# Optimization experiments

Measured on AMD Instinct MI355X. Metric: run time of the kernel, lower is better.

## Reference

```python
import jax, jax.numpy as jnp
import numpy as np

B, N1, N2, C2, K = 8, 2048, 128, 256, 3
D_POS, H0, H1 = 32, 512, 1024


def setup_inputs() -> dict:
    key = jax.random.key(0)
    ks = jax.random.split(key, 14)
    return {
        "xyz1": jax.random.normal(ks[0], (B, N1, 3), jnp.float32),
        "xyz2": jax.random.normal(ks[1], (B, N2, 3), jnp.float32),
        "feat2": jax.random.normal(ks[2], (B, N2, C2), jnp.float32),
        "lrf2": jax.random.normal(ks[3], (B, N2, 3, 3), jnp.float32),
        "w_pos": jax.random.normal(ks[4], (D_POS, 4), jnp.float32) * 0.1,
        "pos_scale": jax.random.uniform(ks[5], (D_POS,), jnp.float32, 0.5, 1.5),
        "pos_bias": jax.random.normal(ks[6], (D_POS,), jnp.float32) * 0.1,
        "w0": jax.random.normal(ks[7], (H0, C2 + D_POS), jnp.float32) * 0.05,
        "s0": jax.random.uniform(ks[8], (H0,), jnp.float32, 0.5, 1.5),
        "b0": jax.random.normal(ks[9], (H0,), jnp.float32) * 0.1,
        "w1": jax.random.normal(ks[10], (H1, H0), jnp.float32) * 0.04,
        "s1": jax.random.uniform(ks[11], (H1,), jnp.float32, 0.5, 1.5),
        "b1": jax.random.normal(ks[12], (H1,), jnp.float32) * 0.1,
        "k": K,
    }


def reference(xyz1, xyz2, feat2, lrf2, w_pos, pos_scale, pos_bias,
              w0, s0, b0, w1, s1, b1, k):
    Bb = xyz1.shape[0]
    # --- get_dists: full pairwise sqrt-distance matrix (B, N1, N2) ---
    d2 = (jnp.sum(xyz1 * xyz1, -1)[:, :, None]
          + jnp.sum(xyz2 * xyz2, -1)[:, None, :]
          - 2.0 * jnp.einsum('bmc,bnc->bmn', xyz1, xyz2))
    dists = jnp.sqrt(jnp.where(d2 < 0, 1e-7, d2))
    # --- k-NN: smallest k in ascending order (== torch.sort then slice) ---
    _, inds = jax.lax.top_k(-dists, k)                    # (B, N1, k)
    bidx = jnp.arange(Bb)[:, None, None]
    feat_nb = feat2[bidx, inds]                           # (B, N1, k, C2)
    close = xyz2[bidx, inds]                              # (B, N1, k, 3)
    lrf_nb = lrf2[bidx, inds]                             # (B, N1, k, 3, 3)
    # --- geometric angle embedding ---
    rel = xyz1[:, :, None, :] - close                     # (B, N1, k, 3)
    rel_norm = jnp.linalg.norm(rel, axis=-1)              # (B, N1, k)
    unit = rel / jnp.maximum(rel_norm, 1e-12)[..., None]  # F.normalize eps
    angle = jnp.einsum('bnkij,bnkj->bnki', lrf_nb, unit)  # (B, N1, k, 3)
    rp = jnp.concatenate([rel_norm[..., None], angle], -1)  # (B, N1, k, 4)
    # --- posembed: 1x1 Conv2d (no bias) + folded BN + LeakyReLU(0.2) ---
    pos = jax.nn.leaky_relu(
        jnp.einsum('bnkc,oc->bnko', rp, w_pos) * pos_scale + pos_bias, 0.2)
    # --- backbone: two 1x1 convs with folded BN + ReLU ---
    x = jnp.concatenate([feat_nb, pos], -1)               # (B, N1, k, C2+32)
    h0 = jax.nn.relu(jnp.einsum('bnkc,oc->bnko', x, w0) * s0 + b0)
    h1 = jax.nn.relu(jnp.einsum('bnkc,oc->bnko', h0, w1) * s1 + b1)
    # --- sum over neighbors, return (B, C_out, N1) like torch ---
    return jnp.transpose(jnp.sum(h1, axis=2), (0, 2, 1))
```

## Files before the change

kernel.cpp:

```cpp
#include <hip/hip_runtime.h>


typedef unsigned short u16;
typedef __bf16 bf16x8 __attribute__((ext_vector_type(8)));
typedef float f32x4 __attribute__((ext_vector_type(4)));
typedef u16 u16x4 __attribute__((ext_vector_type(4)));

#define BQ 8
#define N1Q 2048
#define N2Q 128
#define C2Q 256
#define DPOS 32
#define H0Q 512
#define H1Q 1024
#define NQ (BQ * N1Q)

#define WS_W0F 0u
#define WS_W0P 262144u
#define WS_W1 294912u
#define WS_F2B 1343488u
#define WS_F 1867776u
#define WS_H0 3964928u

__device__ __forceinline__ u16 f2bf(float f) {
  unsigned int u = __builtin_bit_cast(unsigned int, f);
  return (u16)((u + 0x7FFFu + ((u >> 16) & 1u)) >> 16);
}

__device__ __forceinline__ void load16_lds(const void* g, void* l) {
  __builtin_amdgcn_global_load_lds(
      (const __attribute__((address_space(1))) unsigned int*)g,
      (__attribute__((address_space(3))) unsigned int*)l, 16, 0, 0);
}

__global__ void convert_inputs(const float* __restrict__ w0,
                               const float* __restrict__ w1,
                               const float* __restrict__ feat2,
                               u16* __restrict__ w0f, u16* __restrict__ w0p,
                               u16* __restrict__ w1b, u16* __restrict__ f2b) {
  int i = blockIdx.x * 256 + threadIdx.x;
  if (i < 131072) {
    int h = i >> 8, c = i & 255;
    w0f[i] = f2bf(w0[h * 288 + c]);
  } else if (i < 147456) {
    int j = i - 131072;
    int h = j >> 5, c = j & 31;
    w0p[j] = f2bf(w0[h * 288 + 256 + c]);
  } else if (i < 671744) {
    int j = i - 147456;
    w1b[j] = f2bf(w1[j]);
  } else {
    int j = i - 671744;
    f2b[j] = f2bf(feat2[j]);
  }
}

__global__ __launch_bounds__(256, 2) void fgemm(const u16* __restrict__ A,
                                                const u16* __restrict__ W,
                                                float* __restrict__ F) {
  __shared__ alignas(16) u16 As[128 * 32];
  __shared__ alignas(16) u16 Bs[128 * 32];
  const int m0 = (blockIdx.x >> 2) * 128, n0 = (blockIdx.x & 3) * 128;
  const int t = threadIdx.x;
  const int wv = t >> 6, lane = t & 63;
  const int wm = wv >> 1, wn = wv & 1;
  const int quad = lane >> 4, cc = lane & 15;
  const int srow = lane & 15, skc = quad * 8;
  f32x4 acc[4][4] = {};

  for (int k0 = 0; k0 < 256; k0 += 32) {
#pragma unroll
    for (int i = 0; i < 2; i++) {
      int g = i * 4 + wv;
      load16_lds(A + (size_t)(m0 + g * 16 + srow) * 256 + k0 + skc,
                 (char*)As + g * 1024 + (lane << 4));
      load16_lds(W + (size_t)(n0 + g * 16 + srow) * 256 + k0 + skc,
                 (char*)Bs + g * 1024 + (lane << 4));
    }
    __syncthreads();
    bf16x8 af[4], bf[4];
#pragma unroll
    for (int mt = 0; mt < 4; mt++)
      af[mt] = *(const bf16x8*)((const char*)As + (wm * 4 + mt) * 1024 + (lane << 4));
#pragma unroll
    for (int nt = 0; nt < 4; nt++)
      bf[nt] = *(const bf16x8*)((const char*)Bs + (wn * 4 + nt) * 1024 + (lane << 4));
#pragma unroll
    for (int mt = 0; mt < 4; mt++)
#pragma unroll
      for (int nt = 0; nt < 4; nt++)
        acc[mt][nt] = __builtin_amdgcn_mfma_f32_16x16x32_bf16(
            af[mt], bf[nt], acc[mt][nt], 0, 0, 0);
    __syncthreads();
  }

#pragma unroll
  for (int nt = 0; nt < 4; nt++) {
    int gn = n0 + wn * 64 + nt * 16 + cc;
#pragma unroll
    for (int mt = 0; mt < 4; mt++) {
      int gm = m0 + wm * 64 + mt * 16 + quad * 4;
#pragma unroll
      for (int r = 0; r < 4; r++)
        F[(size_t)(gm + r) * H0Q + gn] = acc[mt][nt][r];
    }
  }
}

__global__ __launch_bounds__(256, 2) void build_h0(
    const float* __restrict__ xyz1, const float* __restrict__ xyz2,
    const float* __restrict__ lrf2, const float* __restrict__ w_pos,
    const float* __restrict__ pscale, const float* __restrict__ pbias,
    const u16* __restrict__ w0p, const float* __restrict__ F,
    const float* __restrict__ s0, const float* __restrict__ b0,
    u16* __restrict__ H0) {
  __shared__ float xyz2s[N2Q * 3];
  __shared__ float n2s[N2Q];
  __shared__ float lrfs[N2Q * 9];
  __shared__ float wps[DPOS * 4];
  __shared__ float pss[DPOS];
  __shared__ float pbs[DPOS];
  __shared__ int idxb[192];
  __shared__ float candd[64 * 13];
  __shared__ int candi[64 * 13];
  __shared__ alignas(16) u16 posb[12 * 512];

  const int t = threadIdx.x;
  const int qb = blockIdx.x * 64;
  const int b = qb >> 11;

  for (int i = t; i < N2Q * 3; i += 256) xyz2s[i] = xyz2[b * N2Q * 3 + i];
  for (int i = t; i < N2Q * 9; i += 256) lrfs[i] = lrf2[b * N2Q * 9 + i];
  if (t < DPOS * 4) wps[t] = w_pos[t];
  if (t < DPOS) { pss[t] = pscale[t]; pbs[t] = pbias[t]; }
  __syncthreads();
  if (t < N2Q) {
    float x = xyz2s[t * 3], y = xyz2s[t * 3 + 1], z = xyz2s[t * 3 + 2];
    n2s[t] = x * x + y * y + z * z;
  }
  __syncthreads();

  {
    const int ql = t >> 2, qt = t & 3;
    const int q = qb + ql;
    const float px = xyz1[q * 3], py = xyz1[q * 3 + 1], pz = xyz1[q * 3 + 2];
    const float pn = px * px + py * py + pz * pz;
    float d0 = 1e30f, d1 = 1e30f, d2v = 1e30f;
    int i0 = 0, i1 = 0, i2 = 0;
    const int ibeg = qt * 32;
    for (int i = ibeg; i < ibeg + 32; i++) {
      float dt = px * xyz2s[i * 3] + py * xyz2s[i * 3 + 1] + pz * xyz2s[i * 3 + 2];
      float d = pn + n2s[i] - 2.f * dt;
      if (d < d0) {
        d2v = d1; i2 = i1; d1 = d0; i1 = i0; d0 = d; i0 = i;
      } else if (d < d1) {
        d2v = d1; i2 = i1; d1 = d; i1 = i;
      } else if (d < d2v) {
        d2v = d; i2 = i;
      }
    }
    int base = ql * 13 + qt * 3;
    candd[base] = d0;      candi[base] = i0;
    candd[base + 1] = d1;  candi[base + 1] = i1;
    candd[base + 2] = d2v; candi[base + 2] = i2;
  }
  __syncthreads();

  if (t < 64) {
    float d0 = 1e30f, d1 = 1e30f, d2v = 1e30f;
    int i0 = 0, i1 = 0, i2 = 0;
    int base = t * 13;
#pragma unroll
    for (int c = 0; c < 12; c++) {
      float d = candd[base + c];
      int id = candi[base + c];
      if (d < d0) {
        d2v = d1; i2 = i1; d1 = d0; i1 = i0; d0 = d; i0 = id;
      } else if (d < d1) {
        d2v = d1; i2 = i1; d1 = d; i1 = id;
      } else if (d < d2v) {
        d2v = d; i2 = id;
      }
    }
    idxb[t] = i0;
    idxb[64 + t] = i1;
    idxb[128 + t] = i2;
  }
  __syncthreads();

  if (t < 192) {
    const int ql = t & 63;
    const int q = qb + ql;
    const float px = xyz1[q * 3], py = xyz1[q * 3 + 1], pz = xyz1[q * 3 + 2];
    const int id = idxb[t];
    float rx = px - xyz2s[id * 3];
    float ry = py - xyz2s[id * 3 + 1];
    float rz = pz - xyz2s[id * 3 + 2];
    float rn = sqrtf(rx * rx + ry * ry + rz * rz);
    float inv = 1.f / fmaxf(rn, 1e-12f);
    float ux = rx * inv, uy = ry * inv, uz = rz * inv;
    const float* L = lrfs + id * 9;
    float a0 = L[0] * ux + L[1] * uy + L[2] * uz;
    float a1 = L[3] * ux + L[4] * uy + L[5] * uz;
    float a2 = L[6] * ux + L[7] * uy + L[8] * uz;
    u16* pd = posb + (t >> 4) * 512 + (t & 15) * 8;
#pragma unroll
    for (int o = 0; o < DPOS; o++) {
      float v = wps[o * 4] * rn + wps[o * 4 + 1] * a0 + wps[o * 4 + 2] * a1 +
                wps[o * 4 + 3] * a2;
      v = v * pss[o] + pbs[o];
      v = (v >= 0.f) ? v : 0.2f * v;
      pd[(o >> 3) * 128 + (o & 7)] = f2bf(v);
    }
  }
  __syncthreads();

  const int wv = t >> 6, lane = t & 63;
  const int quad = lane >> 4, cc = lane & 15;
  const float* Fr[3];
  u16* Hr[3];
#pragma unroll
  for (int mt = 0; mt < 3; mt++) {
    int rl = wv * 48 + mt * 16 + cc;
    Fr[mt] = F + ((size_t)(b * N2Q + idxb[rl])) * H0Q;
    int jj = rl >> 6, ql = rl & 63;
    Hr[mt] = H0 + ((size_t)(jj * NQ) + qb + ql) * H0Q;
  }
  bf16x8 afr[3];
#pragma unroll
  for (int mt = 0; mt < 3; mt++)
    afr[mt] = *(const bf16x8*)((const char*)posb + (wv * 3 + mt) * 1024 + (lane << 4));
  const f32x4 zf = {};
  for (int n0 = 0; n0 < H0Q; n0 += 128) {
    bf16x8 bfr[8];
#pragma unroll
    for (int nt = 0; nt < 8; nt++)
      bfr[nt] = *(const bf16x8*)(w0p + (n0 + nt * 16 + cc) * 32 + quad * 8);
    f32x4 acc[3][8];
#pragma unroll
    for (int mt = 0; mt < 3; mt++)
#pragma unroll
      for (int nt = 0; nt < 8; nt++)
        acc[mt][nt] = __builtin_amdgcn_mfma_f32_16x16x32_bf16(bfr[nt], afr[mt],
                                                              zf, 0, 0, 0);
#pragma unroll
    for (int nt = 0; nt < 8; nt++) {
      int hb = n0 + nt * 16 + quad * 4;
      f32x4 sv = *(const f32x4*)(s0 + hb);
      f32x4 bvv = *(const f32x4*)(b0 + hb);
#pragma unroll
      for (int mt = 0; mt < 3; mt++) {
        f32x4 fv = *(const f32x4*)(Fr[mt] + hb);
        u16x4 o4;
#pragma unroll
        for (int r = 0; r < 4; r++) {
          float h = (fv[r] + acc[mt][nt][r]) * sv[r] + bvv[r];
          h = h > 0.f ? h : 0.f;
          o4[r] = f2bf(h);
        }
        *(u16x4*)(Hr[mt] + hb) = o4;
      }
    }
  }
}

__global__ __launch_bounds__(512, 2) void gemm2(const u16* __restrict__ A,
                                                const u16* __restrict__ W,
                                                const float* __restrict__ s,
                                                const float* __restrict__ bz,
                                                float* __restrict__ out) {
  __shared__ alignas(16) u16 As[3][128 * 64];
  __shared__ alignas(16) u16 Bs[3][256 * 64];
  const int id = blockIdx.x;
  const int xcd = id & 7, g = id >> 3;
  const int m0 = (xcd * 16 + (g >> 2)) * 128;
  const int n0 = (g & 3) * 256;
  const int t = threadIdx.x;
  const int wv = t >> 6, lane = t & 63;
  const int wm = wv >> 2, wn = wv & 3;
  const int quad = lane >> 4, cc = lane & 15;
  const int lr = lane & 15, lk = (lane >> 4) * 8;

  const size_t aOff = (size_t)(m0 + wv * 16 + lr) * 512 + lk;
  const size_t bOff = (size_t)(n0 + wv * 32 + lr) * 512 + lk;

  float sv[4], bv[4];
#pragma unroll
  for (int nt = 0; nt < 4; nt++) {
    int gn = n0 + wn * 64 + nt * 16 + cc;
    sv[nt] = s[gn];
    bv[nt] = bz[gn];
  }

  auto stage = [&](int kt, int bi) {
    const u16* Ap = A + (size_t)(kt >> 3) * ((size_t)NQ * H0Q) + ((kt & 7) << 6);
    const u16* Wp = W + ((kt & 7) << 6);
    char* ab = (char*)As[bi] + (lane << 4);
    char* bb = (char*)Bs[bi] + (lane << 4);
    load16_lds(Ap + aOff, ab + wv * 1024);
    load16_lds(Ap + aOff + 32, ab + (8 + wv) * 1024);
    load16_lds(Wp + bOff, bb + (wv * 2) * 1024);
    load16_lds(Wp + bOff + (size_t)16 * 512, bb + (wv * 2 + 1) * 1024);
    load16_lds(Wp + bOff + 32, bb + (16 + wv * 2) * 1024);
    load16_lds(Wp + bOff + (size_t)16 * 512 + 32, bb + (16 + wv * 2 + 1) * 1024);
  };

  f32x4 sum[4][4] = {};
  f32x4 acc[4][4] = {};

  auto tile = [&](int bi, int ktStage) {
    bf16x8 af[2][4], bf[2][4];
    const char* ab = (const char*)As[bi] + (lane << 4);
    const char* bb = (const char*)Bs[bi] + (lane << 4);
#pragma unroll
    for (int kk = 0; kk < 2; kk++)
#pragma unroll
      for (int mt = 0; mt < 4; mt++)
        af[kk][mt] = *(const bf16x8*)(ab + (kk * 8 + wm * 4 + mt) * 1024);
#pragma unroll
    for (int kk = 0; kk < 2; kk++)
#pragma unroll
      for (int nt = 0; nt < 4; nt++)
        bf[kk][nt] = *(const bf16x8*)(bb + (kk * 16 + wn * 4 + nt) * 1024);
    asm volatile("s_waitcnt lgkmcnt(0)" ::: "memory");
    __builtin_amdgcn_s_barrier();
    if (ktStage >= 0) stage(ktStage, bi);
    __builtin_amdgcn_s_setprio(1);
#pragma unroll
    for (int kk = 0; kk < 2; kk++)
#pragma unroll
      for (int mt = 0; mt < 4; mt++)
#pragma unroll
        for (int nt = 0; nt < 4; nt++)
          acc[mt][nt] = __builtin_amdgcn_mfma_f32_16x16x32_bf16(
              af[kk][mt], bf[kk][nt], acc[mt][nt], 0, 0, 0);
    __builtin_amdgcn_s_setprio(0);
  };

  auto fold = [&]() {
#pragma unroll
    for (int mt = 0; mt < 4; mt++)
#pragma unroll
      for (int nt = 0; nt < 4; nt++) {
#pragma unroll
        for (int r = 0; r < 4; r++) {
          float h = acc[mt][nt][r] * sv[nt] + bv[nt];
          sum[mt][nt][r] += (h > 0.f ? h : 0.f);
        }
        acc[mt][nt] = f32x4{};
      }
  };

  stage(0, 0);
  stage(1, 1);
  stage(2, 2);

#pragma unroll 3
  for (int kt = 0; kt < 21; kt++) {
    asm volatile("s_waitcnt vmcnt(12)" ::: "memory");
    __builtin_amdgcn_s_barrier();
    tile(kt % 3, kt + 3);
    if ((kt & 7) == 7) fold();
  }
  asm volatile("s_waitcnt vmcnt(12)" ::: "memory");
  __builtin_amdgcn_s_barrier();
  tile(0, -1);
  asm volatile("s_waitcnt vmcnt(6)" ::: "memory");
  __builtin_amdgcn_s_barrier();
  tile(1, -1);
  asm volatile("s_waitcnt vmcnt(0)" ::: "memory");
  __builtin_amdgcn_s_barrier();
  tile(2, -1);
  fold();

#pragma unroll
  for (int nt = 0; nt < 4; nt++) {
    int gn = n0 + wn * 64 + nt * 16 + cc;
#pragma unroll
    for (int mt = 0; mt < 4; mt++) {
      int gm = m0 + wm * 64 + mt * 16 + quad * 4;
#pragma unroll
      for (int r = 0; r < 4; r++) {
        int q = gm + r;
        out[((size_t)(q >> 11) * H1Q + gn) * N1Q + (q & 2047)] = sum[mt][nt][r];
      }
    }
  }
}

extern "C" void kernel_launch(void* const* d_in, const int* in_sizes, int n_in,
                              void* d_out, int out_size, void* d_ws,
                              size_t ws_size, hipStream_t stream) {
  const float* xyz1 = (const float*)d_in[0];
  const float* xyz2 = (const float*)d_in[1];
  const float* feat2 = (const float*)d_in[2];
  const float* lrf2 = (const float*)d_in[3];
  const float* w_pos = (const float*)d_in[4];
  const float* pscale = (const float*)d_in[5];
  const float* pbias = (const float*)d_in[6];
  const float* w0 = (const float*)d_in[7];
  const float* s0 = (const float*)d_in[8];
  const float* b0 = (const float*)d_in[9];
  const float* w1 = (const float*)d_in[10];
  const float* s1 = (const float*)d_in[11];
  const float* b1 = (const float*)d_in[12];
  float* out = (float*)d_out;

  char* ws = (char*)d_ws;
  u16* w0f = (u16*)(ws + WS_W0F);
  u16* w0p = (u16*)(ws + WS_W0P);
  u16* w1b = (u16*)(ws + WS_W1);
  u16* f2b = (u16*)(ws + WS_F2B);
  float* F = (float*)(ws + WS_F);
  u16* H0 = (u16*)(ws + WS_H0);

  convert_inputs<<<933888 / 256, 256, 0, stream>>>(w0, w1, feat2, w0f, w0p,
                                                   w1b, f2b);
  fgemm<<<32, 256, 0, stream>>>(f2b, w0f, F);
  build_h0<<<NQ / 64, 256, 0, stream>>>(xyz1, xyz2, lrf2, w_pos, pscale,
                                        pbias, w0p, F, s0, b0, H0);
  gemm2<<<512, 512, 0, stream>>>(H0, w1b, s1, b1, out);
}
```

Measured before the change: 231.1 us.

## Split build_h0 across output column blocks and deepen gemm2 pipeline to six stages

```diff
diff --git a/kernel.cpp b/kernel.cpp
--- a/kernel.cpp
+++ b/kernel.cpp
@@ -128,6 +128,7 @@
   const int t = threadIdx.x;
   const int qb = blockIdx.x * 64;
   const int b = qb >> 11;
+  const int n0 = blockIdx.y << 7;
 
   for (int i = t; i < N2Q * 3; i += 256) xyz2s[i] = xyz2[b * N2Q * 3 + i];
   for (int i = t; i < N2Q * 9; i += 256) lrfs[i] = lrf2[b * N2Q * 9 + i];
@@ -231,35 +232,33 @@
   for (int mt = 0; mt < 3; mt++)
     afr[mt] = *(const bf16x8*)((const char*)posb + (wv * 3 + mt) * 1024 + (lane << 4));
   const f32x4 zf = {};
-  for (int n0 = 0; n0 < H0Q; n0 += 128) {
-    bf16x8 bfr[8];
+  bf16x8 bfr[8];
+#pragma unroll
+  for (int nt = 0; nt < 8; nt++)
+    bfr[nt] = *(const bf16x8*)(w0p + (n0 + nt * 16 + cc) * 32 + quad * 8);
+  f32x4 acc[3][8];
+#pragma unroll
+  for (int mt = 0; mt < 3; mt++)
 #pragma unroll
     for (int nt = 0; nt < 8; nt++)
-      bfr[nt] = *(const bf16x8*)(w0p + (n0 + nt * 16 + cc) * 32 + quad * 8);
-    f32x4 acc[3][8];
-#pragma unroll
-    for (int mt = 0; mt < 3; mt++)
-#pragma unroll
-      for (int nt = 0; nt < 8; nt++)
-        acc[mt][nt] = __builtin_amdgcn_mfma_f32_16x16x32_bf16(bfr[nt], afr[mt],
-                                                              zf, 0, 0, 0);
-#pragma unroll
-    for (int nt = 0; nt < 8; nt++) {
-      int hb = n0 + nt * 16 + quad * 4;
-      f32x4 sv = *(const f32x4*)(s0 + hb);
-      f32x4 bvv = *(const f32x4*)(b0 + hb);
-#pragma unroll
-      for (int mt = 0; mt < 3; mt++) {
-        f32x4 fv = *(const f32x4*)(Fr[mt] + hb);
-        u16x4 o4;
-#pragma unroll
-        for (int r = 0; r < 4; r++) {
-          float h = (fv[r] + acc[mt][nt][r]) * sv[r] + bvv[r];
-          h = h > 0.f ? h : 0.f;
-          o4[r] = f2bf(h);
-        }
-        *(u16x4*)(Hr[mt] + hb) = o4;
+      acc[mt][nt] = __builtin_amdgcn_mfma_f32_16x16x32_bf16(bfr[nt], afr[mt],
+                                                            zf, 0, 0, 0);
+#pragma unroll
+  for (int nt = 0; nt < 8; nt++) {
+    int hb = n0 + nt * 16 + quad * 4;
+    f32x4 sv = *(const f32x4*)(s0 + hb);
+    f32x4 bvv = *(const f32x4*)(b0 + hb);
+#pragma unroll
+    for (int mt = 0; mt < 3; mt++) {
+      f32x4 fv = *(const f32x4*)(Fr[mt] + hb);
+      u16x4 o4;
+#pragma unroll
+      for (int r = 0; r < 4; r++) {
+        float h = (fv[r] + acc[mt][nt][r]) * sv[r] + bvv[r];
+        h = h > 0.f ? h : 0.f;
+        o4[r] = f2bf(h);
       }
+      *(u16x4*)(Hr[mt] + hb) = o4;
     }
   }
 }
@@ -269,8 +268,8 @@
                                                 const float* __restrict__ s,
                                                 const float* __restrict__ bz,
                                                 float* __restrict__ out) {
-  __shared__ alignas(16) u16 As[3][128 * 64];
-  __shared__ alignas(16) u16 Bs[3][256 * 64];
+  __shared__ alignas(16) u16 As[6][128 * 32];
+  __shared__ alignas(16) u16 Bs[6][256 * 32];
   const int id = blockIdx.x;
   const int xcd = id & 7, g = id >> 3;
   const int m0 = (xcd * 16 + (g >> 2)) * 128;
@@ -281,59 +280,57 @@
   const int quad = lane >> 4, cc = lane & 15;
   const int lr = lane & 15, lk = (lane >> 4) * 8;
 
-  const size_t aOff = (size_t)(m0 + wv * 16 + lr) * 512 + lk;
-  const size_t bOff = (size_t)(n0 + wv * 32 + lr) * 512 + lk;
-
-  float sv[4], bv[4];
+  const size_t aBase = (size_t)(m0 + wv * 16 + lr) * 512 + lk;
+  const size_t bBase0 = (size_t)(n0 + wv * 32 + lr) * 512 + lk;
+  const size_t bBase1 = bBase0 + (size_t)16 * 512;
+  const int adst = wv * 1024 + (lane << 4);
+  const int bdst0 = (wv * 2) * 1024 + (lane << 4);
+  const int bdst1 = (wv * 2 + 1) * 1024 + (lane << 4);
+
+  f32x4 sv4[4], bv4[4];
 #pragma unroll
   for (int nt = 0; nt < 4; nt++) {
-    int gn = n0 + wn * 64 + nt * 16 + cc;
-    sv[nt] = s[gn];
-    bv[nt] = bz[gn];
-  }
+    int gnb = n0 + wn * 64 + nt * 16 + quad * 4;
+    sv4[nt] = *(const f32x4*)(s + gnb);
+    bv4[nt] = *(const f32x4*)(bz + gnb);
+  }
+#pragma unroll
+  for (int nt = 0; nt < 4; nt++)
+#pragma unroll
+    for (int r = 0; r < 4; r++) {
+      float a = sv4[nt][r], c = bv4[nt][r];
+      asm volatile("" : "+v"(a), "+v"(c));
+      sv4[nt][r] = a; bv4[nt][r] = c;
+    }
 
   auto stage = [&](int kt, int bi) {
-    const u16* Ap = A + (size_t)(kt >> 3) * ((size_t)NQ * H0Q) + ((kt & 7) << 6);
-    const u16* Wp = W + ((kt & 7) << 6);
-    char* ab = (char*)As[bi] + (lane << 4);
-    char* bb = (char*)Bs[bi] + (lane << 4);
-    load16_lds(Ap + aOff, ab + wv * 1024);
-    load16_lds(Ap + aOff + 32, ab + (8 + wv) * 1024);
-    load16_lds(Wp + bOff, bb + (wv * 2) * 1024);
-    load16_lds(Wp + bOff + (size_t)16 * 512, bb + (wv * 2 + 1) * 1024);
-    load16_lds(Wp + bOff + 32, bb + (16 + wv * 2) * 1024);
-    load16_lds(Wp + bOff + (size_t)16 * 512 + 32, bb + (16 + wv * 2 + 1) * 1024);
+    const u16* Ap = A + (size_t)(kt >> 4) * ((size_t)NQ * H0Q) + ((kt & 15) << 5);
+    const u16* Wp = W + ((kt & 15) << 5);
+    load16_lds(Ap + aBase, (char*)As[bi] + adst);
+    load16_lds(Wp + bBase0, (char*)Bs[bi] + bdst0);
+    load16_lds(Wp + bBase1, (char*)Bs[bi] + bdst1);
   };
 
   f32x4 sum[4][4] = {};
   f32x4 acc[4][4] = {};
 
-  auto tile = [&](int bi, int ktStage) {
-    bf16x8 af[2][4], bf[2][4];
+  auto compute = [&](int bi) {
+    bf16x8 af[4], bf[4];
     const char* ab = (const char*)As[bi] + (lane << 4);
     const char* bb = (const char*)Bs[bi] + (lane << 4);
 #pragma unroll
-    for (int kk = 0; kk < 2; kk++)
-#pragma unroll
-      for (int mt = 0; mt < 4; mt++)
-        af[kk][mt] = *(const bf16x8*)(ab + (kk * 8 + wm * 4 + mt) * 1024);
-#pragma unroll
-    for (int kk = 0; kk < 2; kk++)
+    for (int mt = 0; mt < 4; mt++)
+      af[mt] = *(const bf16x8*)(ab + (wm * 4 + mt) * 1024);
+#pragma unroll
+    for (int nt = 0; nt < 4; nt++)
+      bf[nt] = *(const bf16x8*)(bb + (wn * 4 + nt) * 1024);
+    __builtin_amdgcn_s_setprio(1);
+#pragma unroll
+    for (int mt = 0; mt < 4; mt++)
 #pragma unroll
       for (int nt = 0; nt < 4; nt++)
-        bf[kk][nt] = *(const bf16x8*)(bb + (kk * 16 + wn * 4 + nt) * 1024);
-    asm volatile("s_waitcnt lgkmcnt(0)" ::: "memory");
-    __builtin_amdgcn_s_barrier();
-    if (ktStage >= 0) stage(ktStage, bi);
-    __builtin_amdgcn_s_setprio(1);
-#pragma unroll
-    for (int kk = 0; kk < 2; kk++)
-#pragma unroll
-      for (int mt = 0; mt < 4; mt++)
-#pragma unroll
-        for (int nt = 0; nt < 4; nt++)
-          acc[mt][nt] = __builtin_amdgcn_mfma_f32_16x16x32_bf16(
-              af[kk][mt], bf[kk][nt], acc[mt][nt], 0, 0, 0);
+        acc[mt][nt] = __builtin_amdgcn_mfma_f32_16x16x32_bf16(
+            bf[nt], af[mt], acc[mt][nt], 0, 0, 0);
     __builtin_amdgcn_s_setprio(0);
   };
 
@@ -344,45 +341,50 @@
       for (int nt = 0; nt < 4; nt++) {
 #pragma unroll
         for (int r = 0; r < 4; r++) {
-          float h = acc[mt][nt][r] * sv[nt] + bv[nt];
+          float h = acc[mt][nt][r] * sv4[nt][r] + bv4[nt][r];
           sum[mt][nt][r] += (h > 0.f ? h : 0.f);
         }
         acc[mt][nt] = f32x4{};
       }
   };
 
-  stage(0, 0);
-  stage(1, 1);
-  stage(2, 2);
-
-#pragma unroll 3
-  for (int kt = 0; kt < 21; kt++) {
-    asm volatile("s_waitcnt vmcnt(12)" ::: "memory");
+#pragma unroll
+  for (int kt = 0; kt < 5; kt++) stage(kt, kt);
+
+  int bi = 0;
+  for (int kt = 0; kt < 43; kt++) {
     __builtin_amdgcn_s_barrier();
-    tile(kt % 3, kt + 3);
-    if ((kt & 7) == 7) fold();
-  }
-  asm volatile("s_waitcnt vmcnt(12)" ::: "memory");
-  __builtin_amdgcn_s_barrier();
-  tile(0, -1);
-  asm volatile("s_waitcnt vmcnt(6)" ::: "memory");
-  __builtin_amdgcn_s_barrier();
-  tile(1, -1);
-  asm volatile("s_waitcnt vmcnt(0)" ::: "memory");
-  __builtin_amdgcn_s_barrier();
-  tile(2, -1);
+    stage(kt + 5, bi == 0 ? 5 : bi - 1);
+    asm volatile("s_waitcnt vmcnt(15)" ::: "memory");
+    __builtin_amdgcn_s_barrier();
+    compute(bi);
+    if ((kt & 15) == 15) fold();
+    bi = (bi == 5) ? 0 : bi + 1;
+  }
+#define TAILSTEP(VM)                                     \
+  __builtin_amdgcn_s_barrier();                          \
+  asm volatile("s_waitcnt vmcnt(" #VM ")" ::: "memory"); \
+  __builtin_amdgcn_s_barrier();                          \
+  compute(bi);                                           \
+  bi = (bi == 5) ? 0 : bi + 1;
+  TAILSTEP(12)
+  TAILSTEP(9)
+  TAILSTEP(6)
+  TAILSTEP(3)
+  TAILSTEP(0)
+#undef TAILSTEP
   fold();
 
 #pragma unroll
   for (int nt = 0; nt < 4; nt++) {
-    int gn = n0 + wn * 64 + nt * 16 + cc;
 #pragma unroll
     for (int mt = 0; mt < 4; mt++) {
-      int gm = m0 + wm * 64 + mt * 16 + quad * 4;
+      int q = m0 + wm * 64 + mt * 16 + cc;
+      int bb2 = q >> 11, n1 = q & 2047;
 #pragma unroll
       for (int r = 0; r < 4; r++) {
-        int q = gm + r;
-        out[((size_t)(q >> 11) * H1Q + gn) * N1Q + (q & 2047)] = sum[mt][nt][r];
+        int gn = n0 + wn * 64 + nt * 16 + quad * 4 + r;
+        out[((size_t)bb2 * H1Q + gn) * N1Q + n1] = sum[mt][nt][r];
       }
     }
   }
@@ -417,7 +419,8 @@
   convert_inputs<<<933888 / 256, 256, 0, stream>>>(w0, w1, feat2, w0f, w0p,
                                                    w1b, f2b);
   fgemm<<<32, 256, 0, stream>>>(f2b, w0f, F);
-  build_h0<<<NQ / 64, 256, 0, stream>>>(xyz1, xyz2, lrf2, w_pos, pscale,
-                                        pbias, w0p, F, s0, b0, H0);
+  build_h0<<<dim3(NQ / 64, 4), 256, 0, stream>>>(xyz1, xyz2, lrf2, w_pos,
+                                                 pscale, pbias, w0p, F, s0,
+                                                 b0, H0);
   gemm2<<<512, 512, 0, stream>>>(H0, w1b, s1, b1, out);
 }
```

New measurement: 265.0 us. 14.7% more time.

## Retile gemm2 to 64x512 with double buffering and coalesce outputs through LDS

Applied to the files above, without the earlier changes.

```diff
diff --git a/kernel.cpp b/kernel.cpp
--- a/kernel.cpp
+++ b/kernel.cpp
@@ -5,6 +5,7 @@
 typedef __bf16 bf16x8 __attribute__((ext_vector_type(8)));
 typedef float f32x4 __attribute__((ext_vector_type(4)));
 typedef u16 u16x4 __attribute__((ext_vector_type(4)));
+typedef u16 u16x8 __attribute__((ext_vector_type(8)));
 
 #define BQ 8
 #define N1Q 2048
@@ -124,6 +125,7 @@
   __shared__ float candd[64 * 13];
   __shared__ int candi[64 * 13];
   __shared__ alignas(16) u16 posb[12 * 512];
+  __shared__ alignas(16) u16 hstage[192 * 136];
 
   const int t = threadIdx.x;
   const int qb = blockIdx.x * 64;
@@ -218,24 +220,23 @@
   const int wv = t >> 6, lane = t & 63;
   const int quad = lane >> 4, cc = lane & 15;
   const float* Fr[3];
-  u16* Hr[3];
+  int rlv[3];
 #pragma unroll
   for (int mt = 0; mt < 3; mt++) {
     int rl = wv * 48 + mt * 16 + cc;
+    rlv[mt] = rl;
     Fr[mt] = F + ((size_t)(b * N2Q + idxb[rl])) * H0Q;
-    int jj = rl >> 6, ql = rl & 63;
-    Hr[mt] = H0 + ((size_t)(jj * NQ) + qb + ql) * H0Q;
   }
   bf16x8 afr[3];
 #pragma unroll
   for (int mt = 0; mt < 3; mt++)
     afr[mt] = *(const bf16x8*)((const char*)posb + (wv * 3 + mt) * 1024 + (lane << 4));
   const f32x4 zf = {};
-  for (int n0 = 0; n0 < H0Q; n0 += 128) {
+  for (int n0s = 0; n0s < H0Q; n0s += 128) {
     bf16x8 bfr[8];
 #pragma unroll
     for (int nt = 0; nt < 8; nt++)
-      bfr[nt] = *(const bf16x8*)(w0p + (n0 + nt * 16 + cc) * 32 + quad * 8);
+      bfr[nt] = *(const bf16x8*)(w0p + (n0s + nt * 16 + cc) * 32 + quad * 8);
     f32x4 acc[3][8];
 #pragma unroll
     for (int mt = 0; mt < 3; mt++)
@@ -245,7 +246,7 @@
                                                               zf, 0, 0, 0);
 #pragma unroll
     for (int nt = 0; nt < 8; nt++) {
-      int hb = n0 + nt * 16 + quad * 4;
+      int hb = n0s + nt * 16 + quad * 4;
       f32x4 sv = *(const f32x4*)(s0 + hb);
       f32x4 bvv = *(const f32x4*)(b0 + hb);
 #pragma unroll
@@ -258,9 +259,19 @@
           h = h > 0.f ? h : 0.f;
           o4[r] = f2bf(h);
         }
-        *(u16x4*)(Hr[mt] + hb) = o4;
+        *(u16x4*)(hstage + rlv[mt] * 136 + nt * 16 + quad * 4) = o4;
       }
     }
+    __syncthreads();
+#pragma unroll
+    for (int it = 0; it < 12; it++) {
+      int idx = it * 256 + t;
+      int rl = idx >> 4, ch = idx & 15;
+      u16x8 v = *(const u16x8*)(hstage + rl * 136 + ch * 8);
+      int jj = rl >> 6, ql = rl & 63;
+      *(u16x8*)(H0 + ((size_t)(jj * NQ) + qb + ql) * H0Q + n0s + ch * 8) = v;
+    }
+    __syncthreads();
   }
 }
 
@@ -269,73 +280,47 @@
                                                 const float* __restrict__ s,
                                                 const float* __restrict__ bz,
                                                 float* __restrict__ out) {
-  __shared__ alignas(16) u16 As[3][128 * 64];
-  __shared__ alignas(16) u16 Bs[3][256 * 64];
+  __shared__ alignas(16) char smem[147456];
   const int id = blockIdx.x;
-  const int xcd = id & 7, g = id >> 3;
-  const int m0 = (xcd * 16 + (g >> 2)) * 128;
-  const int n0 = (g & 3) * 256;
+  const int xcd = id & 7, ix = id >> 3;
+  const int qt = xcd * 32 + (ix >> 1);
+  const int n0 = (ix & 1) * 512;
+  const int q0 = qt * 64;
   const int t = threadIdx.x;
   const int wv = t >> 6, lane = t & 63;
-  const int wm = wv >> 2, wn = wv & 3;
   const int quad = lane >> 4, cc = lane & 15;
   const int lr = lane & 15, lk = (lane >> 4) * 8;
 
-  const size_t aOff = (size_t)(m0 + wv * 16 + lr) * 512 + lk;
-  const size_t bOff = (size_t)(n0 + wv * 32 + lr) * 512 + lk;
+  const size_t aSrc = (size_t)(q0 + (wv & 3) * 16 + lr) * 512 + (wv >> 2) * 32 + lk;
+  size_t bSrc[4];
+#pragma unroll
+  for (int i = 0; i < 4; i++)
+    bSrc[i] = (size_t)(n0 + (wv * 4 + i) * 16 + lr) * 512 + lk;
+  const int aDst = wv * 1024 + (lane << 4);
 
   float sv[4], bv[4];
 #pragma unroll
   for (int nt = 0; nt < 4; nt++) {
-    int gn = n0 + wn * 64 + nt * 16 + cc;
+    int gn = n0 + wv * 64 + nt * 16 + cc;
     sv[nt] = s[gn];
     bv[nt] = bz[gn];
   }
 
   auto stage = [&](int kt, int bi) {
-    const u16* Ap = A + (size_t)(kt >> 3) * ((size_t)NQ * H0Q) + ((kt & 7) << 6);
-    const u16* Wp = W + ((kt & 7) << 6);
-    char* ab = (char*)As[bi] + (lane << 4);
-    char* bb = (char*)Bs[bi] + (lane << 4);
-    load16_lds(Ap + aOff, ab + wv * 1024);
-    load16_lds(Ap + aOff + 32, ab + (8 + wv) * 1024);
-    load16_lds(Wp + bOff, bb + (wv * 2) * 1024);
-    load16_lds(Wp + bOff + (size_t)16 * 512, bb + (wv * 2 + 1) * 1024);
-    load16_lds(Wp + bOff + 32, bb + (16 + wv * 2) * 1024);
-    load16_lds(Wp + bOff + (size_t)16 * 512 + 32, bb + (16 + wv * 2 + 1) * 1024);
+    const int k0 = (kt & 7) << 6;
+    const u16* Ap = A + (size_t)(kt >> 3) * ((size_t)NQ * H0Q);
+    char* base = smem + bi * 73728;
+    load16_lds(Ap + aSrc + k0, base + aDst);
+#pragma unroll
+    for (int i = 0; i < 4; i++)
+#pragma unroll
+      for (int kk = 0; kk < 2; kk++)
+        load16_lds(W + bSrc[i] + kk * 32 + k0,
+                   base + 8192 + (kk * 32 + wv * 4 + i) * 1024 + (lane << 4));
   };
 
   f32x4 sum[4][4] = {};
   f32x4 acc[4][4] = {};
-
-  auto tile = [&](int bi, int ktStage) {
-    bf16x8 af[2][4], bf[2][4];
-    const char* ab = (const char*)As[bi] + (lane << 4);
-    const char* bb = (const char*)Bs[bi] + (lane << 4);
-#pragma unroll
-    for (int kk = 0; kk < 2; kk++)
-#pragma unroll
-      for (int mt = 0; mt < 4; mt++)
-        af[kk][mt] = *(const bf16x8*)(ab + (kk * 8 + wm * 4 + mt) * 1024);
-#pragma unroll
-    for (int kk = 0; kk < 2; kk++)
-#pragma unroll
-      for (int nt = 0; nt < 4; nt++)
-        bf[kk][nt] = *(const bf16x8*)(bb + (kk * 16 + wn * 4 + nt) * 1024);
-    asm volatile("s_waitcnt lgkmcnt(0)" ::: "memory");
-    __builtin_amdgcn_s_barrier();
-    if (ktStage >= 0) stage(ktStage, bi);
-    __builtin_amdgcn_s_setprio(1);
-#pragma unroll
-    for (int kk = 0; kk < 2; kk++)
-#pragma unroll
-      for (int mt = 0; mt < 4; mt++)
-#pragma unroll
-        for (int nt = 0; nt < 4; nt++)
-          acc[mt][nt] = __builtin_amdgcn_mfma_f32_16x16x32_bf16(
-              af[kk][mt], bf[kk][nt], acc[mt][nt], 0, 0, 0);
-    __builtin_amdgcn_s_setprio(0);
-  };
 
   auto fold = [&]() {
 #pragma unroll
@@ -351,40 +336,67 @@
       }
   };
 
+  auto tile = [&](int kt, bool doStage) {
+    const int bi = kt & 1;
+    const char* base = smem + bi * 73728;
+    bf16x8 af[2][4], bf[2][4];
+#pragma unroll
+    for (int kk = 0; kk < 2; kk++)
+#pragma unroll
+      for (int mt = 0; mt < 4; mt++)
+        af[kk][mt] = *(const bf16x8*)(base + (kk * 4 + mt) * 1024 + (lane << 4));
+#pragma unroll
+    for (int kk = 0; kk < 2; kk++)
+#pragma unroll
+      for (int nt = 0; nt < 4; nt++)
+        bf[kk][nt] = *(const bf16x8*)(base + 8192 + (kk * 32 + wv * 4 + nt) * 1024 +
+                                      (lane << 4));
+    asm volatile("s_waitcnt lgkmcnt(0)" ::: "memory");
+    __builtin_amdgcn_s_barrier();
+    if (doStage) stage(kt + 2, bi);
+    __builtin_amdgcn_s_setprio(1);
+#pragma unroll
+    for (int kk = 0; kk < 2; kk++)
+#pragma unroll
+      for (int mt = 0; mt < 4; mt++)
+#pragma unroll
+        for (int nt = 0; nt < 4; nt++)
+          acc[mt][nt] = __builtin_amdgcn_mfma_f32_16x16x32_bf16(
+              af[kk][mt], bf[kk][nt], acc[mt][nt], 0, 0, 0);
+    __builtin_amdgcn_s_setprio(0);
+  };
+
   stage(0, 0);
   stage(1, 1);
-  stage(2, 2);
-
-#pragma unroll 3
-  for (int kt = 0; kt < 21; kt++) {
-    asm volatile("s_waitcnt vmcnt(12)" ::: "memory");
+
+  for (int kt = 0; kt < 23; kt++) {
+    asm volatile("s_waitcnt vmcnt(9)" ::: "memory");
     __builtin_amdgcn_s_barrier();
-    tile(kt % 3, kt + 3);
+    tile(kt, kt < 22);
     if ((kt & 7) == 7) fold();
   }
-  asm volatile("s_waitcnt vmcnt(12)" ::: "memory");
-  __builtin_amdgcn_s_barrier();
-  tile(0, -1);
-  asm volatile("s_waitcnt vmcnt(6)" ::: "memory");
-  __builtin_amdgcn_s_barrier();
-  tile(1, -1);
   asm volatile("s_waitcnt vmcnt(0)" ::: "memory");
   __builtin_amdgcn_s_barrier();
-  tile(2, -1);
+  tile(23, false);
   fold();
 
-#pragma unroll
-  for (int nt = 0; nt < 4; nt++) {
-    int gn = n0 + wn * 64 + nt * 16 + cc;
-#pragma unroll
-    for (int mt = 0; mt < 4; mt++) {
-      int gm = m0 + wm * 64 + mt * 16 + quad * 4;
-#pragma unroll
-      for (int r = 0; r < 4; r++) {
-        int q = gm + r;
-        out[((size_t)(q >> 11) * H1Q + gn) * N1Q + (q & 2047)] = sum[mt][nt][r];
-      }
-    }
+  float* fs = (float*)smem;
+#pragma unroll
+  for (int mt = 0; mt < 4; mt++)
+#pragma unroll
+    for (int nt = 0; nt < 4; nt++)
+#pragma unroll
+      for (int r = 0; r < 4; r++)
+        fs[(wv * 64 + nt * 16 + cc) * 68 + mt * 16 + quad * 4 + r] =
+            sum[mt][nt][r];
+  __syncthreads();
+  const int bb = q0 >> 11, n1b = q0 & 2047;
+#pragma unroll
+  for (int it = 0; it < 16; it++) {
+    int idx = it * 512 + t;
+    int row = idx >> 4, ch = idx & 15;
+    f32x4 v = *(const f32x4*)(fs + row * 68 + ch * 4);
+    *(f32x4*)(out + ((size_t)(bb * H1Q + n0 + row)) * N1Q + n1b + ch * 4) = v;
   }
 }
 
```

After: 256.8 us. +11.1%, slower.

## Split fused kNN/H0 kernel into separate kNN-pos and H0 MFMA kernels

Applied to the files above, without the earlier changes.

```diff
diff --git a/kernel.cpp b/kernel.cpp
--- a/kernel.cpp
+++ b/kernel.cpp
@@ -5,6 +5,7 @@
 typedef __bf16 bf16x8 __attribute__((ext_vector_type(8)));
 typedef float f32x4 __attribute__((ext_vector_type(4)));
 typedef u16 u16x4 __attribute__((ext_vector_type(4)));
+typedef u16 u16x8 __attribute__((ext_vector_type(8)));
 
 #define BQ 8
 #define N1Q 2048
@@ -21,6 +22,8 @@
 #define WS_F2B 1343488u
 #define WS_F 1867776u
 #define WS_H0 3964928u
+#define WS_POS 54296576u
+#define WS_IDX 57442304u
 
 __device__ __forceinline__ u16 f2bf(float f) {
   unsigned int u = __builtin_bit_cast(unsigned int, f);
@@ -107,30 +110,27 @@
   }
 }
 
-__global__ __launch_bounds__(256, 2) void build_h0(
+__global__ __launch_bounds__(512, 2) void knn_pos(
     const float* __restrict__ xyz1, const float* __restrict__ xyz2,
     const float* __restrict__ lrf2, const float* __restrict__ w_pos,
     const float* __restrict__ pscale, const float* __restrict__ pbias,
-    const u16* __restrict__ w0p, const float* __restrict__ F,
-    const float* __restrict__ s0, const float* __restrict__ b0,
-    u16* __restrict__ H0) {
+    u16* __restrict__ posw, int* __restrict__ idxw) {
   __shared__ float xyz2s[N2Q * 3];
   __shared__ float n2s[N2Q];
   __shared__ float lrfs[N2Q * 9];
   __shared__ float wps[DPOS * 4];
   __shared__ float pss[DPOS];
   __shared__ float pbs[DPOS];
-  __shared__ int idxb[192];
-  __shared__ float candd[64 * 13];
-  __shared__ int candi[64 * 13];
-  __shared__ alignas(16) u16 posb[12 * 512];
+  __shared__ float candd[128 * 13];
+  __shared__ int candi[128 * 13];
+  __shared__ int idxb[384];
 
   const int t = threadIdx.x;
-  const int qb = blockIdx.x * 64;
+  const int qb = blockIdx.x * 128;
   const int b = qb >> 11;
 
-  for (int i = t; i < N2Q * 3; i += 256) xyz2s[i] = xyz2[b * N2Q * 3 + i];
-  for (int i = t; i < N2Q * 9; i += 256) lrfs[i] = lrf2[b * N2Q * 9 + i];
+  for (int i = t; i < N2Q * 3; i += 512) xyz2s[i] = xyz2[b * N2Q * 3 + i];
+  for (int i = t; i < N2Q * 9; i += 512) lrfs[i] = lrf2[b * N2Q * 9 + i];
   if (t < DPOS * 4) wps[t] = w_pos[t];
   if (t < DPOS) { pss[t] = pscale[t]; pbs[t] = pbias[t]; }
   __syncthreads();
@@ -166,7 +166,7 @@
   }
   __syncthreads();
 
-  if (t < 64) {
+  if (t < 128) {
     float d0 = 1e30f, d1 = 1e30f, d2v = 1e30f;
     int i0 = 0, i1 = 0, i2 = 0;
     int base = t * 13;
@@ -183,16 +183,16 @@
       }
     }
     idxb[t] = i0;
-    idxb[64 + t] = i1;
-    idxb[128 + t] = i2;
+    idxb[128 + t] = i1;
+    idxb[256 + t] = i2;
   }
   __syncthreads();
 
-  if (t < 192) {
-    const int ql = t & 63;
+  if (t < 384) {
+    const int j = t >> 7, ql = t & 127;
     const int q = qb + ql;
     const float px = xyz1[q * 3], py = xyz1[q * 3 + 1], pz = xyz1[q * 3 + 2];
-    const int id = idxb[t];
+    const int id = idxb[j * 128 + ql];
     float rx = px - xyz2s[id * 3];
     float ry = py - xyz2s[id * 3 + 1];
     float rz = pz - xyz2s[id * 3 + 2];
@@ -203,64 +203,61 @@
     float a0 = L[0] * ux + L[1] * uy + L[2] * uz;
     float a1 = L[3] * ux + L[4] * uy + L[5] * uz;
     float a2 = L[6] * ux + L[7] * uy + L[8] * uz;
-    u16* pd = posb + (t >> 4) * 512 + (t & 15) * 8;
-#pragma unroll
-    for (int o = 0; o < DPOS; o++) {
-      float v = wps[o * 4] * rn + wps[o * 4 + 1] * a0 + wps[o * 4 + 2] * a1 +
-                wps[o * 4 + 3] * a2;
-      v = v * pss[o] + pbs[o];
-      v = (v >= 0.f) ? v : 0.2f * v;
-      pd[(o >> 3) * 128 + (o & 7)] = f2bf(v);
-    }
-  }
-  __syncthreads();
-
+    const size_t row = (size_t)j * NQ + q;
+    idxw[row] = id;
+#pragma unroll
+    for (int c = 0; c < 4; c++) {
+      u16x8 chunk;
+#pragma unroll
+      for (int e = 0; e < 8; e++) {
+        int o = c * 8 + e;
+        float v = wps[o * 4] * rn + wps[o * 4 + 1] * a0 + wps[o * 4 + 2] * a1 +
+                  wps[o * 4 + 3] * a2;
+        v = v * pss[o] + pbs[o];
+        v = (v >= 0.f) ? v : 0.2f * v;
+        chunk[e] = f2bf(v);
+      }
+      *(u16x8*)(posw + row * 32 + c * 8) = chunk;
+    }
+  }
+}
+
+__global__ __launch_bounds__(256, 4) void h0_kernel(
+    const u16* __restrict__ posw, const int* __restrict__ idxw,
+    const u16* __restrict__ w0p, const float* __restrict__ F,
+    const float* __restrict__ s0, const float* __restrict__ b0,
+    u16* __restrict__ H0) {
+  const int t = threadIdx.x;
   const int wv = t >> 6, lane = t & 63;
   const int quad = lane >> 4, cc = lane & 15;
-  const float* Fr[3];
-  u16* Hr[3];
-#pragma unroll
-  for (int mt = 0; mt < 3; mt++) {
-    int rl = wv * 48 + mt * 16 + cc;
-    Fr[mt] = F + ((size_t)(b * N2Q + idxb[rl])) * H0Q;
-    int jj = rl >> 6, ql = rl & 63;
-    Hr[mt] = H0 + ((size_t)(jj * NQ) + qb + ql) * H0Q;
-  }
-  bf16x8 afr[3];
-#pragma unroll
-  for (int mt = 0; mt < 3; mt++)
-    afr[mt] = *(const bf16x8*)((const char*)posb + (wv * 3 + mt) * 1024 + (lane << 4));
+  const int r0 = (blockIdx.x * 4 + wv) * 16;
+
+  const int r = r0 + cc;
+  const int q = r & (NQ - 1);
+  const int bb = q >> 11;
+  const int idv = idxw[r];
+  const float* Fr = F + ((size_t)(bb * N2Q + idv)) * H0Q;
+  u16* Hr = H0 + (size_t)r * H0Q;
+
+  const bf16x8 afr = *(const bf16x8*)(posw + (size_t)r * 32 + quad * 8);
   const f32x4 zf = {};
-  for (int n0 = 0; n0 < H0Q; n0 += 128) {
-    bf16x8 bfr[8];
-#pragma unroll
-    for (int nt = 0; nt < 8; nt++)
-      bfr[nt] = *(const bf16x8*)(w0p + (n0 + nt * 16 + cc) * 32 + quad * 8);
-    f32x4 acc[3][8];
-#pragma unroll
-    for (int mt = 0; mt < 3; mt++)
-#pragma unroll
-      for (int nt = 0; nt < 8; nt++)
-        acc[mt][nt] = __builtin_amdgcn_mfma_f32_16x16x32_bf16(bfr[nt], afr[mt],
-                                                              zf, 0, 0, 0);
-#pragma unroll
-    for (int nt = 0; nt < 8; nt++) {
-      int hb = n0 + nt * 16 + quad * 4;
-      f32x4 sv = *(const f32x4*)(s0 + hb);
-      f32x4 bvv = *(const f32x4*)(b0 + hb);
-#pragma unroll
-      for (int mt = 0; mt < 3; mt++) {
-        f32x4 fv = *(const f32x4*)(Fr[mt] + hb);
-        u16x4 o4;
-#pragma unroll
-        for (int r = 0; r < 4; r++) {
-          float h = (fv[r] + acc[mt][nt][r]) * sv[r] + bvv[r];
-          h = h > 0.f ? h : 0.f;
-          o4[r] = f2bf(h);
-        }
-        *(u16x4*)(Hr[mt] + hb) = o4;
-      }
-    }
+
+#pragma unroll 4
+  for (int nt = 0; nt < 32; nt++) {
+    const bf16x8 bfr = *(const bf16x8*)(w0p + (nt * 16 + cc) * 32 + quad * 8);
+    f32x4 acc = __builtin_amdgcn_mfma_f32_16x16x32_bf16(bfr, afr, zf, 0, 0, 0);
+    const int hb = nt * 16 + quad * 4;
+    const f32x4 sv = *(const f32x4*)(s0 + hb);
+    const f32x4 bv = *(const f32x4*)(b0 + hb);
+    const f32x4 fv = *(const f32x4*)(Fr + hb);
+    u16x4 o4;
+#pragma unroll
+    for (int e = 0; e < 4; e++) {
+      float h = (fv[e] + acc[e]) * sv[e] + bv[e];
+      h = h > 0.f ? h : 0.f;
+      o4[e] = f2bf(h);
+    }
+    *(u16x4*)(Hr + hb) = o4;
   }
 }
 
@@ -413,11 +410,14 @@
   u16* f2b = (u16*)(ws + WS_F2B);
   float* F = (float*)(ws + WS_F);
   u16* H0 = (u16*)(ws + WS_H0);
+  u16* posw = (u16*)(ws + WS_POS);
+  int* idxw = (int*)(ws + WS_IDX);
 
   convert_inputs<<<933888 / 256, 256, 0, stream>>>(w0, w1, feat2, w0f, w0p,
                                                    w1b, f2b);
   fgemm<<<32, 256, 0, stream>>>(f2b, w0f, F);
-  build_h0<<<NQ / 64, 256, 0, stream>>>(xyz1, xyz2, lrf2, w_pos, pscale,
-                                        pbias, w0p, F, s0, b0, H0);
+  knn_pos<<<128, 512, 0, stream>>>(xyz1, xyz2, lrf2, w_pos, pscale, pbias,
+                                   posw, idxw);
+  h0_kernel<<<768, 256, 0, stream>>>(posw, idxw, w0p, F, s0, b0, H0);
   gemm2<<<512, 512, 0, stream>>>(H0, w1b, s1, b1, out);
 }
```

New measurement: 234.9 us. About the same (+1.7%).
